# Kernel tuning notes

Hardware: AMD Instinct MI355X
Metric: run time of the kernel (lower is better)

## Reference

```python
import jax, jax.numpy as jnp
import numpy as np
import math

B, S, D = 32, 4096, 1024


def setup_inputs() -> dict:
    key = jax.random.key(0)
    k1, k2, k3 = jax.random.split(key, 3)
    return {
        "query": jax.random.normal(k1, (B, D), dtype=jnp.float32),
        "key": jax.random.normal(k2, (B, S, D), dtype=jnp.float32),
        "value": jax.random.normal(k3, (B, S, D), dtype=jnp.float32),
        "attn_mask": jnp.ones((B, S), dtype=jnp.int32),
    }


def reference(query, key, value, attn_mask):
    # query: [B, D] -> treated as single-query attention over S keys.
    d = query.shape[-1]
    scale = 1.0 / math.sqrt(d)
    # attn: [B, S]  (the torch code's [B, 1, S] with the singleton squeezed)
    attn = jnp.einsum("bd,bsd->bs", query, key) * scale
    attn = jnp.where(attn_mask == 0, -jnp.inf, attn)
    weights = jax.nn.softmax(attn, axis=-1)
    # dropout(p=0.1) is identity in eval mode; omitted for determinism
    result = jnp.einsum("bs,bsd->bd", weights, value)
    return result[:, None, :]  # [B, 1, D], matching torch output shape
```

## Files before the change

kernel.cpp:

```cpp
#include <hip/hip_runtime.h>
#include <math.h>

#define BB 32
#define SS 4096
#define DD 1024
#define CHUNKS 32
#define CHUNK_S (SS / CHUNKS)
#define SCALE 0.03125f

__global__ __launch_bounds__(256) void attn_partial(
    const float* __restrict__ q,
    const float* __restrict__ k,
    const float* __restrict__ v,
    const int*   __restrict__ mask,
    float* __restrict__ part_o,
    float* __restrict__ part_ml)
{
    const int c    = blockIdx.x;
    const int b    = blockIdx.y;
    const int tid  = threadIdx.x;
    const int lane = tid & 63;
    const int wave = tid >> 6;

    __shared__ float s_scores[CHUNK_S];
    __shared__ float s_w[CHUNK_S];

    const float* qb = q + (size_t)b * DD;
    float4 qf[4];
#pragma unroll
    for (int j = 0; j < 4; ++j)
        qf[j] = *(const float4*)(qb + 4 * lane + 256 * j);

    const int s0 = c * CHUNK_S;

    for (int it = 0; it < CHUNK_S / 4; ++it) {
        const int i    = wave + 4 * it;
        const int srow = s0 + i;
        const float* krow = k + ((size_t)b * SS + srow) * DD;
        float acc = 0.f;
#pragma unroll
        for (int j = 0; j < 4; ++j) {
            float4 kf = *(const float4*)(krow + 4 * lane + 256 * j);
            acc += qf[j].x * kf.x + qf[j].y * kf.y + qf[j].z * kf.z + qf[j].w * kf.w;
        }
#pragma unroll
        for (int off = 32; off > 0; off >>= 1)
            acc += __shfl_xor(acc, off, 64);
        if (lane == 0) {
            float sc = acc * SCALE;
            if (mask[(size_t)b * SS + srow] == 0) sc = -1e30f;
            s_scores[i] = sc;
        }
    }
    __syncthreads();

    float m = -1e30f;
#pragma unroll 8
    for (int i = 0; i < CHUNK_S; ++i) m = fmaxf(m, s_scores[i]);
    if (tid < CHUNK_S) s_w[tid] = expf(s_scores[tid] - m);
    __syncthreads();
    float l = 0.f;
#pragma unroll 8
    for (int i = 0; i < CHUNK_S; ++i) l += s_w[i];

    const float* vb = v + ((size_t)b * SS + s0) * DD + 4 * tid;
    float4 acc = {0.f, 0.f, 0.f, 0.f};
    for (int i = 0; i < CHUNK_S; ++i) {
        const float w  = s_w[i];
        const float4 vf = *(const float4*)(vb + (size_t)i * DD);
        acc.x += w * vf.x;
        acc.y += w * vf.y;
        acc.z += w * vf.z;
        acc.w += w * vf.w;
    }
    *(float4*)(part_o + ((size_t)b * CHUNKS + c) * DD + 4 * tid) = acc;
    if (tid == 0) {
        part_ml[((size_t)b * CHUNKS + c) * 2 + 0] = m;
        part_ml[((size_t)b * CHUNKS + c) * 2 + 1] = l;
    }
}

__global__ __launch_bounds__(256) void attn_combine(
    const float* __restrict__ part_o,
    const float* __restrict__ part_ml,
    float* __restrict__ out)
{
    const int b   = blockIdx.x;
    const int tid = threadIdx.x;

    __shared__ float s_m[CHUNKS];
    __shared__ float s_l[CHUNKS];
    __shared__ float s_scale[CHUNKS];

    if (tid < CHUNKS) {
        s_m[tid] = part_ml[((size_t)b * CHUNKS + tid) * 2 + 0];
        s_l[tid] = part_ml[((size_t)b * CHUNKS + tid) * 2 + 1];
    }
    __syncthreads();

    float m = -1e30f;
#pragma unroll
    for (int c = 0; c < CHUNKS; ++c) m = fmaxf(m, s_m[c]);
    if (tid < CHUNKS) s_scale[tid] = expf(s_m[tid] - m);
    __syncthreads();

    float L = 0.f;
#pragma unroll
    for (int c = 0; c < CHUNKS; ++c) L += s_l[c] * s_scale[c];
    const float inv_L = 1.f / L;

    float4 acc = {0.f, 0.f, 0.f, 0.f};
    for (int c = 0; c < CHUNKS; ++c) {
        const float sc = s_scale[c];
        const float4 o = *(const float4*)(part_o + ((size_t)b * CHUNKS + c) * DD + 4 * tid);
        acc.x += sc * o.x;
        acc.y += sc * o.y;
        acc.z += sc * o.z;
        acc.w += sc * o.w;
    }
    acc.x *= inv_L; acc.y *= inv_L; acc.z *= inv_L; acc.w *= inv_L;
    *(float4*)(out + (size_t)b * DD + 4 * tid) = acc;
}

extern "C" void kernel_launch(void* const* d_in, const int* in_sizes, int n_in,
                              void* d_out, int out_size, void* d_ws, size_t ws_size,
                              hipStream_t stream) {
    const float* q    = (const float*)d_in[0];
    const float* k    = (const float*)d_in[1];
    const float* v    = (const float*)d_in[2];
    const int*   mask = (const int*)d_in[3];
    float* out = (float*)d_out;

    float* part_o  = (float*)d_ws;
    float* part_ml = part_o + (size_t)BB * CHUNKS * DD;

    dim3 grid1(CHUNKS, BB);
    attn_partial<<<grid1, 256, 0, stream>>>(q, k, v, mask, part_o, part_ml);
    attn_combine<<<BB, 256, 0, stream>>>(part_o, part_ml, out);
}
```

Baseline: 968.1 us.

## Fuse score and value passes into per-wave online softmax with mask skipping

Each wave now processes a contiguous slice of keys, computing each score and immediately accumulating the weighted value row with an online-softmax rescale. The four per-wave partial results are merged through shared memory. This removes the separate score phase, the block-wide barriers and the serial max/sum loops over shared scores, and it overlaps K and V streaming. Rows whose mask is zero are skipped entirely. The cost is extra registers for the accumulators, a data-dependent branch per row and 16KB of shared memory per block.

```diff
diff --git a/kernel.cpp b/kernel.cpp
--- a/kernel.cpp
+++ b/kernel.cpp
@@ -6,6 +6,7 @@
 #define DD 1024
 #define CHUNKS 32
 #define CHUNK_S (SS / CHUNKS)
+#define KPW (CHUNK_S / 4)
 #define SCALE 0.03125f
 
 __global__ __launch_bounds__(256) void attn_partial(
@@ -22,8 +23,13 @@
     const int lane = tid & 63;
     const int wave = tid >> 6;
 
-    __shared__ float s_scores[CHUNK_S];
-    __shared__ float s_w[CHUNK_S];
+    __shared__ float s_o[4 * DD];
+    __shared__ float s_m[4], s_l[4];
+    __shared__ int   s_mask[CHUNK_S];
+
+    const int s0 = c * CHUNK_S;
+
+    if (tid < CHUNK_S) s_mask[tid] = mask[(size_t)b * SS + s0 + tid];
 
     const float* qb = q + (size_t)b * DD;
     float4 qf[4];
@@ -31,52 +37,77 @@
     for (int j = 0; j < 4; ++j)
         qf[j] = *(const float4*)(qb + 4 * lane + 256 * j);
 
-    const int s0 = c * CHUNK_S;
-
-    for (int it = 0; it < CHUNK_S / 4; ++it) {
-        const int i    = wave + 4 * it;
-        const int srow = s0 + i;
-        const float* krow = k + ((size_t)b * SS + srow) * DD;
-        float acc = 0.f;
-#pragma unroll
-        for (int j = 0; j < 4; ++j) {
-            float4 kf = *(const float4*)(krow + 4 * lane + 256 * j);
-            acc += qf[j].x * kf.x + qf[j].y * kf.y + qf[j].z * kf.z + qf[j].w * kf.w;
-        }
-#pragma unroll
-        for (int off = 32; off > 0; off >>= 1)
-            acc += __shfl_xor(acc, off, 64);
-        if (lane == 0) {
-            float sc = acc * SCALE;
-            if (mask[(size_t)b * SS + srow] == 0) sc = -1e30f;
-            s_scores[i] = sc;
-        }
-    }
     __syncthreads();
 
+    const size_t base = ((size_t)b * SS + s0 + wave * KPW) * DD;
+    const float* kp = k + base + 4 * lane;
+    const float* vp = v + base + 4 * lane;
+
     float m = -1e30f;
-#pragma unroll 8
-    for (int i = 0; i < CHUNK_S; ++i) m = fmaxf(m, s_scores[i]);
-    if (tid < CHUNK_S) s_w[tid] = expf(s_scores[tid] - m);
+    float l = 0.f;
+    float4 o[4] = {{0,0,0,0},{0,0,0,0},{0,0,0,0},{0,0,0,0}};
+
+#pragma unroll 2
+    for (int i = 0; i < KPW; ++i) {
+        if (s_mask[wave * KPW + i] != 0) {
+            float acc = 0.f;
+#pragma unroll
+            for (int j = 0; j < 4; ++j) {
+                float4 kf = *(const float4*)(kp + 256 * j);
+                acc += qf[j].x * kf.x + qf[j].y * kf.y + qf[j].z * kf.z + qf[j].w * kf.w;
+            }
+#pragma unroll
+            for (int off = 32; off > 0; off >>= 1)
+                acc += __shfl_xor(acc, off, 64);
+            const float sc = acc * SCALE;
+
+            if (sc > m) {
+                const float alpha = __expf(m - sc);
+                l *= alpha;
+#pragma unroll
+                for (int j = 0; j < 4; ++j) {
+                    o[j].x *= alpha; o[j].y *= alpha;
+                    o[j].z *= alpha; o[j].w *= alpha;
+                }
+                m = sc;
+            }
+            const float w = __expf(sc - m);
+            l += w;
+#pragma unroll
+            for (int j = 0; j < 4; ++j) {
+                const float4 vf = *(const float4*)(vp + 256 * j);
+                o[j].x += w * vf.x; o[j].y += w * vf.y;
+                o[j].z += w * vf.z; o[j].w += w * vf.w;
+            }
+        }
+        kp += DD; vp += DD;
+    }
+
+#pragma unroll
+    for (int j = 0; j < 4; ++j)
+        *(float4*)(s_o + wave * DD + 4 * lane + 256 * j) = o[j];
+    if (lane == 0) { s_m[wave] = m; s_l[wave] = l; }
     __syncthreads();
-    float l = 0.f;
-#pragma unroll 8
-    for (int i = 0; i < CHUNK_S; ++i) l += s_w[i];
 
-    const float* vb = v + ((size_t)b * SS + s0) * DD + 4 * tid;
+    float M = fmaxf(fmaxf(s_m[0], s_m[1]), fmaxf(s_m[2], s_m[3]));
+    float e[4];
+#pragma unroll
+    for (int w = 0; w < 4; ++w) e[w] = __expf(s_m[w] - M);
+    float L = 0.f;
+#pragma unroll
+    for (int w = 0; w < 4; ++w) L += e[w] * s_l[w];
+
     float4 acc = {0.f, 0.f, 0.f, 0.f};
-    for (int i = 0; i < CHUNK_S; ++i) {
-        const float w  = s_w[i];
-        const float4 vf = *(const float4*)(vb + (size_t)i * DD);
-        acc.x += w * vf.x;
-        acc.y += w * vf.y;
-        acc.z += w * vf.z;
-        acc.w += w * vf.w;
+#pragma unroll
+    for (int w = 0; w < 4; ++w) {
+        const float4 ow = *(const float4*)(s_o + w * DD + 4 * tid);
+        acc.x += e[w] * ow.x; acc.y += e[w] * ow.y;
+        acc.z += e[w] * ow.z; acc.w += e[w] * ow.w;
     }
     *(float4*)(part_o + ((size_t)b * CHUNKS + c) * DD + 4 * tid) = acc;
     if (tid == 0) {
-        part_ml[((size_t)b * CHUNKS + c) * 2 + 0] = m;
-        part_ml[((size_t)b * CHUNKS + c) * 2 + 1] = l;
+        part_ml[((size_t)b * CHUNKS + c) * 2 + 0] = M;
+        part_ml[((size_t)b * CHUNKS + c) * 2 + 1] = L;
     }
 }
 
@@ -101,7 +132,7 @@
     float m = -1e30f;
 #pragma unroll
     for (int c = 0; c < CHUNKS; ++c) m = fmaxf(m, s_m[c]);
-    if (tid < CHUNKS) s_scale[tid] = expf(s_m[tid] - m);
+    if (tid < CHUNKS) s_scale[tid] = __expf(s_m[tid] - m);
     __syncthreads();
 
     float L = 0.f;
```

Result: no change. 986.5 us (+1.9%).
